# Kernel optimization log

Hardware: AMD Instinct MI355X
Metric: run time of the kernel (lower is better)

## Reference

```python
import jax, jax.numpy as jnp
import numpy as np
import math

PHI = (1 + math.sqrt(5)) / 2
B, T, D, H = 2, 2048, 1024, 16
DH = D // H
DC = 1024
DFF = int(D * PHI)  # 1657


def setup_inputs() -> dict:
    key = jax.random.key(0)
    ks = jax.random.split(key, 16)
    n = lambda i, shape, s=0.02: jax.random.normal(ks[i], shape, jnp.float32) * s
    tril = jnp.tril(jnp.ones((T, T), bool))
    mask = jnp.where(tril, 0.0, -1e9).astype(jnp.float32)[None, None]  # causal additive
    return dict(
        x=jax.random.normal(ks[0], (B, T, D), jnp.float32),
        center_from_above=jax.random.normal(ks[1], (B, DC), jnp.float32),
        mask=mask,
        gate_w=n(2, (D, 1), 0.5), gate_b=jnp.zeros((1,), jnp.float32),
        cb_w=n(3, (DC, 1), 0.5),
        nf_g=jnp.ones((D,), jnp.float32), nf_b=jnp.zeros((D,), jnp.float32),
        wq=n(4, (D, D)), wk=n(5, (D, D)), wv=n(6, (D, D)), wo=n(7, (D, D)),
        phase=jnp.linspace(0.0, math.pi, H).astype(jnp.float32),
        nb_g=jnp.ones((D,), jnp.float32), nb_b=jnp.zeros((D,), jnp.float32),
        up_w=n(8, (D, DFF)), up_b=jnp.zeros((DFF,), jnp.float32),
        dn_w=n(9, (DFF, D)), dn_b=jnp.zeros((D,), jnp.float32),
        commit_w=n(10, (D, 1)), commit_b=jnp.zeros((1,), jnp.float32),
        cproj_w=n(11, (D, DC)), cproj_b=jnp.zeros((DC,), jnp.float32),
        bcast_w=n(12, (DC, D)), bcast_b=jnp.zeros((D,), jnp.float32),
    )


def _ln(x, g, b, eps=1e-5):
    m = x.mean(-1, keepdims=True)
    v = ((x - m) ** 2).mean(-1, keepdims=True)
    return (x - m) * jax.lax.rsqrt(v + eps) * g + b


def _forward(x, center_from_above, mask, gate_w, gate_b, cb_w, nf_g, nf_b,
             wq, wk, wv, wo, phase, nb_g, nb_b, up_w, up_b, dn_w, dn_b,
             commit_w, commit_b, cproj_w, cproj_b, bcast_w, bcast_b):
    # broadcast center from above into the field
    x = x + (center_from_above @ bcast_w + bcast_b)[:, None, :]
    # binary aperture with straight-through estimator
    logits = x @ gate_w + gate_b + (center_from_above @ cb_w)[:, None, :]  # (B,T,1)
    prob = jax.nn.sigmoid(logits)
    hard = (prob > 0.5).astype(x.dtype)
    gate = hard - jax.lax.stop_gradient(prob) + prob
    h = _ln(x, nf_g, nf_b)
    heads = lambda w: (h @ w).reshape(B, T, H, DH).transpose(0, 2, 1, 3)  # (B,H,T,DH)
    Q, K, V = heads(wq), heads(wk), heads(wv)
    half = DH // 2
    c = jnp.cos(phase)[None, :, None, None]
    s = jnp.sin(phase)[None, :, None, None]
    def rot(z):
        re, im = z[..., :half], z[..., half:]
        return jnp.concatenate([re * c - im * s, re * s + im * c], axis=-1)
    Q, K = rot(Q), rot(K)
    ge = gate[:, None]  # (B,1,T,1)
    Q = Q * ge
    K = K * ge
    scores = jnp.einsum('bhqd,bhkd->bhqk', Q, K) / math.sqrt(DH) + mask
    attn = jax.nn.softmax(scores, axis=-1)
    fo = jnp.einsum('bhqk,bhkd->bhqd', attn, V).transpose(0, 2, 1, 3).reshape(B, T, D)
    fo = (fo @ wo) * gate
    x = x + fo
    h2 = _ln(x, nb_g, nb_b)
    ff = jax.nn.gelu(h2 @ up_w + up_b, approximate=False) @ dn_w + dn_b
    center_pool = x.mean(axis=1)  # (B,D)
    commit = jax.nn.sigmoid(center_pool @ commit_w + commit_b)  # (B,1)
    x = x + commit[:, None, :] * gate * ff
    center = jnp.tanh(center_pool @ cproj_w + cproj_b)  # (B,DC)
    return x, center, gate, commit


def reference(x, center_from_above, mask, gate_w, gate_b, cb_w, nf_g, nf_b,
              wq, wk, wv, wo, phase, nb_g, nb_b, up_w, up_b, dn_w, dn_b,
              commit_w, commit_b, cproj_w, cproj_b, bcast_w, bcast_b):
    return _forward(x, center_from_above, mask, gate_w, gate_b, cb_w, nf_g, nf_b,
                    wq, wk, wv, wo, phase, nb_g, nb_b, up_w, up_b, dn_w, dn_b,
                    commit_w, commit_b, cproj_w, cproj_b, bcast_w, bcast_b)
```

## Files before the change

### kernel.cpp

```cpp
#include <hip/hip_runtime.h>
#include <math.h>

#define B_   2
#define T_   2048
#define D_   1024
#define H_   16
#define DH_  64
#define DC_  1024
#define DFF_ 1656
#define DFFP_ 1664
#define MTOT 4096
#define NELEM_X 4194304ull

typedef short s16x8 __attribute__((ext_vector_type(8)));
typedef unsigned short u16x4 __attribute__((ext_vector_type(4)));
typedef float f32x4 __attribute__((ext_vector_type(4)));
typedef float f32x16 __attribute__((ext_vector_type(16)));
typedef unsigned short bfbits;

__device__ __forceinline__ bfbits f2bf(float f) {
  unsigned int u = __builtin_bit_cast(unsigned int, f);
  u += 0x7fffu + ((u >> 16) & 1u);
  return (bfbits)(u >> 16);
}

__device__ __forceinline__ float vexp2(float x) {
  float r;
  asm("v_exp_f32 %0, %1" : "=v"(r) : "v"(x));
  return r;
}
__device__ __forceinline__ unsigned pkbf(float lo, float hi) {
  unsigned r;
  asm("v_cvt_pk_bf16_f32 %0, %1, %2" : "=v"(r) : "v"(lo), "v"(hi));
  return r;
}

__device__ __forceinline__ void gload16(const void* g, void* l) {
  __builtin_amdgcn_global_load_lds(
      (__attribute__((address_space(1))) void*)g,
      (__attribute__((address_space(3))) void*)l, 16, 0, 0);
}

constexpr size_t OFF_X1   = 0;
constexpr size_t OFF_H    = OFF_X1 + 4ull*NELEM_X;
constexpr size_t OFF_Q    = OFF_H  + 2ull*NELEM_X;
constexpr size_t OFF_K    = OFF_Q  + 2ull*NELEM_X;
constexpr size_t OFF_VT   = OFF_K  + 2ull*NELEM_X;
constexpr size_t OFF_AO   = OFF_VT + 2ull*NELEM_X;
constexpr size_t OFF_X2   = OFF_AO + 2ull*NELEM_X;
constexpr size_t OFF_WQKV = OFF_X2 + 4ull*NELEM_X;
constexpr size_t OFF_WO   = OFF_WQKV + 3072ull*1024*2;
constexpr size_t OFF_WUP  = OFF_WO   + 1024ull*1024*2;
constexpr size_t OFF_WDN  = OFF_WUP  + 1664ull*1024*2;
constexpr size_t OFF_BVEC = OFF_WDN  + 1024ull*1664*2;
constexpr size_t OFF_CBV  = OFF_BVEC + 2048ull*4;
constexpr size_t OFF_GATE = OFF_CBV  + 256;
constexpr size_t OFF_PART = OFF_GATE + 4096ull*4;
constexpr size_t OFF_POOL = OFF_PART + 128ull*1024*4;
constexpr size_t OFF_CMT  = OFF_POOL + 2048ull*4;
constexpr size_t OFF_PM   = OFF_CMT  + 256;
constexpr size_t OFF_PL   = OFF_PM   + 1024ull*64*4;

__constant__ unsigned short JOBS[8][6] = {
  {0x00F, 0x11C, 0x11A, 0x118, 0x006, 0x000},
  {0x11E, 0x11D, 0x11B, 0x119, 0x005, 0x001},
  {0x11F, 0x21D, 0x21B, 0x219, 0x004, 0x002},
  {0x21F, 0x21C, 0x00B, 0x114, 0x008, 0x003},
  {0x21E, 0x00C, 0x116, 0x009, 0x007, 0x210},
  {0x00E, 0x117, 0x217, 0x110, 0x111, 0x211},
  {0x00D, 0x218, 0x115, 0x112, 0x213, 0x212},
  {0x21A, 0x215, 0x216, 0x00A, 0x113, 0x214},
};

__global__ __launch_bounds__(256)
void transpose_w(const float* __restrict__ src, bfbits* __restrict__ dst,
                 int R, int C, int Rpad, int Npad) {
  __shared__ float tile[32][33];
  const int kb = blockIdx.x * 32, nb = blockIdx.y * 32;
  const int tx = threadIdx.x & 31, ty = threadIdx.x >> 5;
  for (int i = ty; i < 32; i += 8) {
    const int k = kb + i, n = nb + tx;
    tile[i][tx] = (k < R && n < C) ? src[(size_t)k * C + n] : 0.f;
  }
  __syncthreads();
  for (int i = ty; i < 32; i += 8) {
    const int n = nb + i, k = kb + tx;
    if (n < Npad && k < Rpad) dst[(size_t)n * Rpad + k] = f2bf(tile[tx][i]);
  }
}

__global__ __launch_bounds__(256)
void gemv_t(const float* __restrict__ v, const float* __restrict__ w,
            const float* __restrict__ bias, float* __restrict__ out,
            int tanh_mode) {
  const int b = blockIdx.y;
  const int dl = threadIdx.x & 31, cl = threadIdx.x >> 5;
  const int d = blockIdx.x * 32 + dl;
  const float* vb = v + b * 1024;
  float s = 0.f;
  #pragma unroll 4
  for (int c = cl; c < 1024; c += 8)
    s += vb[c] * w[(size_t)c * 1024 + d];
  __shared__ float red[8][32];
  red[cl][dl] = s;
  __syncthreads();
  if (threadIdx.x < 32) {
    float t = 0.f;
    #pragma unroll
    for (int i = 0; i < 8; ++i) t += red[i][threadIdx.x];
    const int dd = blockIdx.x * 32 + threadIdx.x;
    t += bias[dd];
    out[b * 1024 + dd] = tanh_mode ? tanhf(t) : t;
  }
}

__global__ __launch_bounds__(256)
void cb_kernel(const float* __restrict__ cfa, const float* __restrict__ cbw,
               float* __restrict__ cbv) {
  const int b = blockIdx.x, tid = threadIdx.x;
  float4 a = *(const float4*)(cfa + b * 1024 + tid * 4);
  float4 w = *(const float4*)(cbw + tid * 4);
  float s = a.x * w.x + a.y * w.y + a.z * w.z + a.w * w.w;
  #pragma unroll
  for (int o = 32; o > 0; o >>= 1) s += __shfl_xor(s, o);
  __shared__ float ls[4];
  if ((tid & 63) == 0) ls[tid >> 6] = s;
  __syncthreads();
  if (tid == 0) cbv[b] = ls[0] + ls[1] + ls[2] + ls[3];
}

__device__ __forceinline__ void blockreduce3(float& a, float& b, float& c) {
  #pragma unroll
  for (int o = 32; o > 0; o >>= 1) {
    a += __shfl_xor(a, o);
    b += __shfl_xor(b, o);
    c += __shfl_xor(c, o);
  }
  __shared__ float ls[3][4];
  const int lane = threadIdx.x & 63, w = threadIdx.x >> 6;
  if (lane == 0) { ls[0][w] = a; ls[1][w] = b; ls[2][w] = c; }
  __syncthreads();
  a = ls[0][0] + ls[0][1] + ls[0][2] + ls[0][3];
  b = ls[1][0] + ls[1][1] + ls[1][2] + ls[1][3];
  c = ls[2][0] + ls[2][1] + ls[2][2] + ls[2][3];
}

__global__ __launch_bounds__(256)
void ln1_kernel(const float* __restrict__ x, const float* __restrict__ bvec,
                const float* __restrict__ cbv, const float* __restrict__ gw,
                const float* __restrict__ gb, const float* __restrict__ nfg,
                const float* __restrict__ nfb, float* __restrict__ x1,
                bfbits* __restrict__ h, float* __restrict__ gate_ws,
                float* __restrict__ gate_out) {
  const int m = blockIdx.x, tid = threadIdx.x, b = m >> 11;
  const size_t ro = (size_t)m * D_ + tid * 4;
  float4 xv = *(const float4*)(x + ro);
  float4 bv = *(const float4*)(bvec + b * D_ + tid * 4);
  float4 v;
  v.x = xv.x + bv.x; v.y = xv.y + bv.y; v.z = xv.z + bv.z; v.w = xv.w + bv.w;
  float4 g4 = *(const float4*)(gw + tid * 4);
  float s  = v.x + v.y + v.z + v.w;
  float s2 = v.x*v.x + v.y*v.y + v.z*v.z + v.w*v.w;
  float dg = v.x*g4.x + v.y*g4.y + v.z*g4.z + v.w*g4.w;
  blockreduce3(s, s2, dg);
  const float mean = s * (1.0f/1024.0f);
  const float var  = s2 * (1.0f/1024.0f) - mean*mean;
  const float rstd = rsqrtf(var + 1e-5f);
  if (tid == 0) {
    const float logits = dg + gb[0] + cbv[b];
    const float prob = 1.0f / (1.0f + expf(-logits));
    const float hard = prob > 0.5f ? 1.0f : 0.0f;
    const float gv = (hard - prob) + prob;
    gate_ws[m] = gv; gate_out[m] = gv;
  }
  *(float4*)(x1 + ro) = v;
  float4 gg = *(const float4*)(nfg + tid * 4);
  float4 b2 = *(const float4*)(nfb + tid * 4);
  u16x4 hv;
  hv[0] = f2bf((v.x - mean) * rstd * gg.x + b2.x);
  hv[1] = f2bf((v.y - mean) * rstd * gg.y + b2.y);
  hv[2] = f2bf((v.z - mean) * rstd * gg.z + b2.z);
  hv[3] = f2bf((v.w - mean) * rstd * gg.w + b2.w);
  *(u16x4*)(h + ro) = hv;
}

__global__ __launch_bounds__(256)
void ln2_kernel(const float* __restrict__ x2, const float* __restrict__ gptr,
                const float* __restrict__ bptr, bfbits* __restrict__ h2) {
  const int m = blockIdx.x, tid = threadIdx.x;
  const size_t ro = (size_t)m * D_ + tid * 4;
  float4 v = *(const float4*)(x2 + ro);
  float s  = v.x + v.y + v.z + v.w;
  float s2 = v.x*v.x + v.y*v.y + v.z*v.z + v.w*v.w;
  float d0 = 0.f;
  blockreduce3(s, s2, d0);
  const float mean = s * (1.0f/1024.0f);
  const float var  = s2 * (1.0f/1024.0f) - mean*mean;
  const float rstd = rsqrtf(var + 1e-5f);
  float4 gg = *(const float4*)(gptr + tid * 4);
  float4 b2 = *(const float4*)(bptr + tid * 4);
  u16x4 hv;
  hv[0] = f2bf((v.x - mean) * rstd * gg.x + b2.x);
  hv[1] = f2bf((v.y - mean) * rstd * gg.y + b2.y);
  hv[2] = f2bf((v.z - mean) * rstd * gg.z + b2.z);
  hv[3] = f2bf((v.w - mean) * rstd * gg.w + b2.w);
  *(u16x4*)(h2 + ro) = hv;
}

template <int EPI, int BM, int BK, int BN>
__global__ void __launch_bounds__(256, 2)
gemm_bt(const bfbits* __restrict__ A, int lda,
        const bfbits* __restrict__ Bt, int ldb, int K,
        const float* __restrict__ p0, const float* __restrict__ p1,
        const float* __restrict__ p2,
        float* __restrict__ fo0, const float* __restrict__ fo1,
        bfbits* __restrict__ bo0, bfbits* __restrict__ bo1,
        bfbits* __restrict__ bo2) {
  constexpr int MI = BM / 32;
  constexpr int NJ = BN / 32;
  constexpr int RCH = BK / 8;
  constexpr int NK = BK / 32;
  __shared__ bfbits Asl[2][BM * BK];
  __shared__ bfbits Bsl[2][BN * BK];
  const int tid = threadIdx.x;
  const int lane = tid & 63, wave = tid >> 6;
  const int g = lane >> 4, l15 = lane & 15;
  const int wr = wave >> 1, wc = wave & 1;
  const int m0 = blockIdx.y * BM, n0 = blockIdx.x * BN;

  auto stage = [&](int k0, int p) {
    #pragma unroll
    for (int i = 0; i < (BM * RCH) / 256; ++i) {
      const int c = i * 256 + tid;
      const int row = c / RCH;
      const int ko = ((c % RCH) ^ (row & (RCH - 1))) * 8;
      gload16(A + (size_t)(m0 + row) * lda + (k0 + ko),
              (char*)&Asl[p][0] + c * 16);
    }
    #pragma unroll
    for (int i = 0; i < (BN * RCH) / 256; ++i) {
      const int c = i * 256 + tid;
      const int row = c / RCH;
      const int ko = ((c % RCH) ^ (row & (RCH - 1))) * 8;
      gload16(Bt + (size_t)(n0 + row) * ldb + (k0 + ko),
              (char*)&Bsl[p][0] + c * 16);
    }
  };

  f32x4 acc[MI][NJ] = {};
  stage(0, 0);
  __syncthreads();

  int t = 0;
  for (int k0 = 0; k0 < K; k0 += BK, ++t) {
    const int p = t & 1;
    if (k0 + BK < K) stage(k0 + BK, p ^ 1);
    s16x8 af[NK][MI], bfr[NK][NJ];
    #pragma unroll
    for (int kk = 0; kk < NK; ++kk) {
      #pragma unroll
      for (int i = 0; i < MI; ++i) {
        const int row = wr * (MI * 16) + i * 16 + l15;
        af[kk][i] = *(const s16x8*)&Asl[p][row * BK + (((kk * 4 + g) ^ (row & (RCH - 1))) * 8)];
      }
      #pragma unroll
      for (int i = 0; i < NJ; ++i) {
        const int row = wc * (NJ * 16) + i * 16 + l15;
        bfr[kk][i] = *(const s16x8*)&Bsl[p][row * BK + (((kk * 4 + g) ^ (row & (RCH - 1))) * 8)];
      }
    }
    #pragma unroll
    for (int kk = 0; kk < NK; ++kk)
      #pragma unroll
      for (int i = 0; i < MI; ++i)
        #pragma unroll
        for (int j = 0; j < NJ; ++j)
          acc[i][j] = __builtin_amdgcn_mfma_f32_16x16x32_bf16(af[kk][i], bfr[kk][j], acc[i][j], 0, 0, 0);
    __syncthreads();
  }

  const int b = m0 >> 11;
  const int trow0 = (m0 & 2047) + wr * (MI * 16);

  if constexpr (EPI == 0) {
    const float* gate = p0;
    const float* phase = p1;
    const int ncol0 = n0 + wc * 64;
    const int section = ncol0 >> 10;
    const int hh = (ncol0 & 1023) >> 6;
    if (section == 2) {
      bfbits* vt = bo2;
      const size_t vhead = (size_t)(b * H_ + hh) * DH_ * T_;
      #pragma unroll
      for (int mi = 0; mi < MI; ++mi) {
        const int tb = trow0 + mi * 16 + g * 4;
        #pragma unroll
        for (int ni = 0; ni < NJ; ++ni) {
          const int dh = ni * 16 + l15;
          unsigned* dst32 = (unsigned*)&vt[vhead + (size_t)dh * T_ + tb];
          dst32[0] = pkbf(acc[mi][ni][0], acc[mi][ni][1]);
          dst32[1] = pkbf(acc[mi][ni][2], acc[mi][ni][3]);
        }
      }
    } else {
      const float cc = cosf(phase[hh]);
      const float ssn = sinf(phase[hh]);
      const float qs = (section == 0) ? 0.125f * 1.44269504088896341f : 1.0f;
      bfbits* dst = (section == 0) ? bo0 : bo1;
      const size_t head = (size_t)(b * H_ + hh) * T_ * DH_;
      #pragma unroll
      for (int mi = 0; mi < MI; ++mi) {
        const int tb = trow0 + mi * 16 + g * 4;
        float gv[4];
        #pragma unroll
        for (int r = 0; r < 4; ++r) gv[r] = gate[(size_t)b * T_ + tb + r] * qs;
        #pragma unroll
        for (int ni = 0; ni < 2; ++ni) {
          const int dh = ni * 16 + l15;
          #pragma unroll
          for (int r = 0; r < 4; ++r) {
            const float re = acc[mi][ni][r];
            const float im = acc[mi][ni + 2][r];
            const size_t idx = head + (size_t)(tb + r) * DH_ + dh;
            dst[idx]      = f2bf((re * cc - im * ssn) * gv[r]);
            dst[idx + 32] = f2bf((re * ssn + im * cc) * gv[r]);
          }
        }
      }
    }
  } else if constexpr (EPI == 1) {
    const float* gate = p0;
    const float* x1 = fo1;
    float* x2 = fo0;
    #pragma unroll
    for (int mi = 0; mi < MI; ++mi) {
      const int m = m0 + wr * (MI * 16) + mi * 16 + g * 4;
      float gv[4];
      #pragma unroll
      for (int r = 0; r < 4; ++r) gv[r] = gate[m + r];
      #pragma unroll
      for (int ni = 0; ni < NJ; ++ni) {
        const int n = n0 + wc * (NJ * 16) + ni * 16 + l15;
        #pragma unroll
        for (int r = 0; r < 4; ++r) {
          const size_t idx = (size_t)(m + r) * D_ + n;
          x2[idx] = x1[idx] + acc[mi][ni][r] * gv[r];
        }
      }
    }
  } else if constexpr (EPI == 2) {
    const float* upb = p0;
    bfbits* outm = bo0;
    #pragma unroll
    for (int mi = 0; mi < MI; ++mi) {
      const int m = m0 + wr * (MI * 16) + mi * 16 + g * 4;
      #pragma unroll
      for (int ni = 0; ni < NJ; ++ni) {
        const int n = n0 + wc * (NJ * 16) + ni * 16 + l15;
        const float bb = upb[n < DFF_ ? n : DFF_ - 1];
        #pragma unroll
        for (int r = 0; r < 4; ++r) {
          float v = acc[mi][ni][r] + bb;
          v = 0.5f * v * (1.0f + erff(v * 0.70710678118654752f));
          outm[(size_t)(m + r) * DFFP_ + n] = f2bf(v);
        }
      }
    }
  } else {
    const float* dnb = p0;
    const float* gate = p1;
    const float* cmt = p2;
    const float* x2 = fo1;
    float* outx = fo0;
    const float cb = cmt[b];
    #pragma unroll
    for (int mi = 0; mi < MI; ++mi) {
      const int m = m0 + wr * (MI * 16) + mi * 16 + g * 4;
      float kv[4];
      #pragma unroll
      for (int r = 0; r < 4; ++r) kv[r] = cb * gate[m + r];
      #pragma unroll
      for (int ni = 0; ni < NJ; ++ni) {
        const int n = n0 + wc * (NJ * 16) + ni * 16 + l15;
        const float bb = dnb[n];
        #pragma unroll
        for (int r = 0; r < 4; ++r) {
          const size_t idx = (size_t)(m + r) * D_ + n;
          outx[idx] = x2[idx] + kv[r] * (acc[mi][ni][r] + bb);
        }
      }
    }
  }
}

__global__ void __launch_bounds__(128, 3)
attn_kernel(const bfbits* __restrict__ Qb, const bfbits* __restrict__ Kb,
            const bfbits* __restrict__ Vt, bfbits* __restrict__ AO,
            float* __restrict__ pm, float* __restrict__ pl,
            float* __restrict__ pO) {
  __shared__ bfbits Kl[64 * 64];
  __shared__ bfbits Vl[64 * 64];
  const int pid = blockIdx.x;
  const int bh = pid & 31;
  const int j = (pid >> 5) & 7;
  const int slot = pid >> 8;
  const unsigned job = JOBS[j][slot];
  const int qt = job & 0xFF;
  const int kind = job >> 8;
  const int nk = qt + 1;
  const int mid = (nk + 1) >> 1;
  const int t0 = (kind == 2) ? mid : 0;
  const int t1 = (kind == 1) ? mid : nk;
  const int qb0 = qt * 64;
  const int tid = threadIdx.x, lane = tid & 63, wq = tid >> 6;
  const int l31 = lane & 31, hi = lane >> 5;
  const int qw = qb0 + wq * 32;

  const bfbits* Qp = Qb + ((size_t)bh * T_ + qw) * DH_;
  const bfbits* Kp = Kb + (size_t)bh * T_ * DH_;
  const bfbits* Vp = Vt + (size_t)bh * DH_ * T_;

  s16x8 qf[4];
  #pragma unroll
  for (int mf = 0; mf < 4; ++mf)
    qf[mf] = *(const s16x8*)(Qp + l31 * DH_ + mf * 16 + hi * 8);

  f32x16 o0 = {}, o1 = {};
  float mrun = -INFINITY, lrun = 0.f;

  const bfbits* kg[4];
  const bfbits* vg[4];
  int cb_[4];
  #pragma unroll
  for (int i = 0; i < 4; ++i) {
    const int c = i * 128 + tid;
    const int row = c >> 3;
    const int sc = ((c & 7) ^ (row & 7)) * 8;
    kg[i] = Kp + row * DH_ + sc;
    vg[i] = Vp + (size_t)row * T_ + sc;
    cb_[i] = c * 16;
  }

  for (int t = t0; t < t1; ++t) {
    const int k0 = t << 6;
    #pragma unroll
    for (int i = 0; i < 4; ++i) {
      gload16(kg[i] + (size_t)k0 * DH_, (char*)&Kl[0] + cb_[i]);
      gload16(vg[i] + k0,               (char*)&Vl[0] + cb_[i]);
    }
    __syncthreads();
    f32x16 s0 = {}, s1 = {};
    __builtin_amdgcn_s_setprio(1);
    #pragma unroll
    for (int mf = 0; mf < 4; ++mf) {
      const int ch = ((mf * 2 + hi) ^ (l31 & 7)) * 8;
      const s16x8 ka  = *(const s16x8*)&Kl[l31 * 64 + ch];
      const s16x8 kb2 = *(const s16x8*)&Kl[(32 + l31) * 64 + ch];
      s0 = __builtin_amdgcn_mfma_f32_32x32x16_bf16(ka,  qf[mf], s0, 0, 0, 0);
      s1 = __builtin_amdgcn_mfma_f32_32x32x16_bf16(kb2, qf[mf], s1, 0, 0, 0);
    }
    __builtin_amdgcn_s_setprio(0);
    if (t == qt) {
      const int qd = wq * 32 + l31;
      #pragma unroll
      for (int r = 0; r < 16; ++r) {
        const int krow = (r & 3) + 8 * (r >> 2) + 4 * hi;
        if (krow > qd)      s0[r] = -1e9f;
        if (krow + 32 > qd) s1[r] = -1e9f;
      }
    }
    float red[8];
    #pragma unroll
    for (int i = 0; i < 8; ++i)
      red[i] = fmaxf(fmaxf(s0[i], s0[i + 8]), fmaxf(s1[i], s1[i + 8]));
    #pragma unroll
    for (int i = 0; i < 4; ++i) red[i] = fmaxf(red[i], red[i + 4]);
    float mx = fmaxf(fmaxf(red[0], red[1]), fmaxf(red[2], red[3]));
    mx = fmaxf(mx, __shfl_xor(mx, 32));
    const bool need = __any(mx > mrun + 8.f) != 0;
    const float mnew = need ? fmaxf(mrun, mx) : mrun;
    s0 = s0 - mnew;
    s1 = s1 - mnew;
    #pragma unroll
    for (int i = 0; i < 16; ++i) { s0[i] = vexp2(s0[i]); s1[i] = vexp2(s1[i]); }
    float sr[8];
    #pragma unroll
    for (int i = 0; i < 8; ++i)
      sr[i] = (s0[i] + s0[i + 8]) + (s1[i] + s1[i + 8]);
    #pragma unroll
    for (int i = 0; i < 4; ++i) sr[i] += sr[i + 4];
    float sum = (sr[0] + sr[1]) + (sr[2] + sr[3]);
    sum += __shfl_xor(sum, 32);
    if (need) {
      const float alpha = vexp2(mrun - mnew);
      mrun = mnew;
      lrun = lrun * alpha + sum;
      o0 *= alpha;
      o1 *= alpha;
    } else {
      lrun += sum;
    }
    #pragma unroll
    for (int mf = 0; mf < 4; ++mf) {
      const f32x16& s = (mf < 2) ? s0 : s1;
      const int r0 = (mf & 1) * 8;
      const unsigned A0 = pkbf(s[r0 + 0], s[r0 + 1]);
      const unsigned A1 = pkbf(s[r0 + 2], s[r0 + 3]);
      const unsigned B0 = pkbf(s[r0 + 4], s[r0 + 5]);
      const unsigned B1 = pkbf(s[r0 + 6], s[r0 + 7]);
      const unsigned x0 = (unsigned)__shfl_xor((int)(hi ? A0 : B0), 32);
      const unsigned x1 = (unsigned)__shfl_xor((int)(hi ? A1 : B1), 32);
      uint4 wv;
      wv.x = hi ? x0 : A0;
      wv.y = hi ? x1 : A1;
      wv.z = hi ? B0 : x0;
      wv.w = hi ? B1 : x1;
      const s16x8 pf = __builtin_bit_cast(s16x8, wv);
      const int ch = ((mf * 2 + hi) ^ (l31 & 7)) * 8;
      const s16x8 v0 = *(const s16x8*)&Vl[l31 * 64 + ch];
      const s16x8 v1 = *(const s16x8*)&Vl[(32 + l31) * 64 + ch];
      __builtin_amdgcn_s_setprio(1);
      o0 = __builtin_amdgcn_mfma_f32_32x32x16_bf16(v0, pf, o0, 0, 0, 0);
      o1 = __builtin_amdgcn_mfma_f32_32x32x16_bf16(v1, pf, o1, 0, 0, 0);
      __builtin_amdgcn_s_setprio(0);
    }
    __syncthreads();
  }

  if (kind == 0) {
    const float inv = 1.0f / lrun;
    const int q = qw + l31;
    bfbits* dst = AO + ((size_t)(bh >> 4) * T_ + q) * D_ + (bh & 15) * DH_;
    #pragma unroll
    for (int rp = 0; rp < 8; ++rp) {
      const int dh = ((2 * rp) & 3) + 8 * (rp >> 1) + 4 * hi;
      *(unsigned*)(dst + dh)      = pkbf(o0[2 * rp] * inv, o0[2 * rp + 1] * inv);
      *(unsigned*)(dst + 32 + dh) = pkbf(o1[2 * rp] * inv, o1[2 * rp + 1] * inv);
    }
  } else {
    const int jid = ((qt - 16) * 32 + bh) * 2 + (kind - 1);
    const int qloc = wq * 32 + l31;
    pm[jid * 64 + qloc] = mrun;
    pl[jid * 64 + qloc] = lrun;
    float* po = pO + (size_t)jid * 4096;
    #pragma unroll
    for (int r = 0; r < 16; ++r) {
      const int dh = (r & 3) + 8 * (r >> 2) + 4 * hi;
      po[dh * 64 + qloc]        = o0[r];
      po[(dh + 32) * 64 + qloc] = o1[r];
    }
  }
}

__global__ void __launch_bounds__(64)
attn_merge(const float* __restrict__ pm, const float* __restrict__ pl,
           const float* __restrict__ pO, bfbits* __restrict__ AO) {
  __shared__ float lds[64][65];
  const int u = blockIdx.x;
  const int qt = 16 + (u >> 5), bh = u & 31;
  const int q = threadIdx.x;
  const int jA = ((qt - 16) * 32 + bh) * 2, jB = jA + 1;
  const float mA = pm[jA * 64 + q], mB = pm[jB * 64 + q];
  const float lA = pl[jA * 64 + q], lB = pl[jB * 64 + q];
  const float m = fmaxf(mA, mB);
  const float eA = vexp2(mA - m), eB = vexp2(mB - m);
  const float inv = 1.0f / (lA * eA + lB * eB);
  const float* OA = pO + (size_t)jA * 4096;
  const float* OB = pO + (size_t)jB * 4096;
  for (int dh = 0; dh < 64; ++dh)
    lds[dh][q] = (OA[dh * 64 + q] * eA + OB[dh * 64 + q] * eB) * inv;
  __syncthreads();
  const int b = bh >> 4, hh = bh & 15;
  bfbits* dst = AO + ((size_t)b * T_ + qt * 64) * D_ + hh * DH_ + q;
  for (int qq = 0; qq < 64; ++qq)
    dst[(size_t)qq * D_] = f2bf(lds[q][qq]);
}

__global__ __launch_bounds__(256)
void pool_part(const float* __restrict__ x2, float* __restrict__ part) {
  const int s = blockIdx.x, b = blockIdx.y, tid = threadIdx.x;
  const float* base = x2 + ((size_t)b * T_ + s * 32) * D_ + tid * 4;
  float ax = 0, ay = 0, az = 0, aw = 0;
  #pragma unroll 4
  for (int t = 0; t < 32; ++t) {
    float4 v = *(const float4*)(base + (size_t)t * D_);
    ax += v.x; ay += v.y; az += v.z; aw += v.w;
  }
  float4 ov; ov.x = ax; ov.y = ay; ov.z = az; ov.w = aw;
  *(float4*)(part + (size_t)(b * 64 + s) * D_ + tid * 4) = ov;
}

__global__ __launch_bounds__(256)
void pool_fin(const float* __restrict__ part, float* __restrict__ pool) {
  const int idx = blockIdx.x * 256 + threadIdx.x;
  const int b = idx >> 10, d = idx & 1023;
  float s = 0.f;
  #pragma unroll 8
  for (int i = 0; i < 64; ++i) s += part[(size_t)(b * 64 + i) * D_ + d];
  pool[idx] = s * (1.0f / 2048.0f);
}

__global__ __launch_bounds__(256)
void commit_kernel(const float* __restrict__ pool, const float* __restrict__ cw,
                   const float* __restrict__ cb0, float* __restrict__ cmt,
                   float* __restrict__ out_cmt) {
  const int b = blockIdx.x, tid = threadIdx.x;
  float4 p = *(const float4*)(pool + b * 1024 + tid * 4);
  float4 w = *(const float4*)(cw + tid * 4);
  float s = p.x * w.x + p.y * w.y + p.z * w.z + p.w * w.w;
  #pragma unroll
  for (int o = 32; o > 0; o >>= 1) s += __shfl_xor(s, o);
  __shared__ float ls[4];
  if ((tid & 63) == 0) ls[tid >> 6] = s;
  __syncthreads();
  if (tid == 0) {
    const float t = ls[0] + ls[1] + ls[2] + ls[3] + cb0[0];
    const float v = 1.0f / (1.0f + expf(-t));
    cmt[b] = v; out_cmt[b] = v;
  }
}

extern "C" void kernel_launch(void* const* d_in, const int* in_sizes, int n_in,
                              void* d_out, int out_size, void* d_ws, size_t ws_size,
                              hipStream_t stream) {
  (void)in_sizes; (void)n_in; (void)out_size; (void)ws_size;
  const float* x       = (const float*)d_in[0];
  const float* cfa     = (const float*)d_in[1];
  const float* gate_w  = (const float*)d_in[3];
  const float* gate_b  = (const float*)d_in[4];
  const float* cb_w    = (const float*)d_in[5];
  const float* nf_g    = (const float*)d_in[6];
  const float* nf_b    = (const float*)d_in[7];
  const float* wq      = (const float*)d_in[8];
  const float* wk      = (const float*)d_in[9];
  const float* wv      = (const float*)d_in[10];
  const float* wo      = (const float*)d_in[11];
  const float* phase   = (const float*)d_in[12];
  const float* nb_g    = (const float*)d_in[13];
  const float* nb_b    = (const float*)d_in[14];
  const float* up_w    = (const float*)d_in[15];
  const float* up_b    = (const float*)d_in[16];
  const float* dn_w    = (const float*)d_in[17];
  const float* dn_b    = (const float*)d_in[18];
  const float* cmt_w   = (const float*)d_in[19];
  const float* cmt_b   = (const float*)d_in[20];
  const float* cproj_w = (const float*)d_in[21];
  const float* cproj_b = (const float*)d_in[22];
  const float* bcast_w = (const float*)d_in[23];
  const float* bcast_b = (const float*)d_in[24];

  char* ws = (char*)d_ws;
  float*  x1     = (float*)(ws + OFF_X1);
  bfbits* h      = (bfbits*)(ws + OFF_H);
  bfbits* h2     = (bfbits*)(ws + OFF_H);
  bfbits* qb     = (bfbits*)(ws + OFF_Q);
  bfbits* kb     = (bfbits*)(ws + OFF_K);
  bfbits* vt     = (bfbits*)(ws + OFF_VT);
  bfbits* ffmid  = (bfbits*)(ws + OFF_Q);
  bfbits* ao     = (bfbits*)(ws + OFF_AO);
  float*  x2     = (float*)(ws + OFF_X2);
  float*  pO     = (float*)(ws + OFF_X2);
  bfbits* wqkv_t = (bfbits*)(ws + OFF_WQKV);
  bfbits* wo_t   = (bfbits*)(ws + OFF_WO);
  bfbits* wup_t  = (bfbits*)(ws + OFF_WUP);
  bfbits* wdn_t  = (bfbits*)(ws + OFF_WDN);
  float*  bvec   = (float*)(ws + OFF_BVEC);
  float*  cbv    = (float*)(ws + OFF_CBV);
  float*  gate   = (float*)(ws + OFF_GATE);
  float*  part   = (float*)(ws + OFF_PART);
  float*  pool   = (float*)(ws + OFF_POOL);
  float*  cmt    = (float*)(ws + OFF_CMT);
  float*  pm     = (float*)(ws + OFF_PM);
  float*  pl     = (float*)(ws + OFF_PL);

  float* outx   = (float*)d_out;
  float* outc   = outx + NELEM_X;
  float* outg   = outc + B_ * DC_;
  float* outcmt = outg + B_ * T_;

  transpose_w<<<dim3(32, 32), 256, 0, stream>>>(wq, wqkv_t,                1024, 1024, 1024, 1024);
  transpose_w<<<dim3(32, 32), 256, 0, stream>>>(wk, wqkv_t + 1024 * 1024,  1024, 1024, 1024, 1024);
  transpose_w<<<dim3(32, 32), 256, 0, stream>>>(wv, wqkv_t + 2048 * 1024,  1024, 1024, 1024, 1024);
  transpose_w<<<dim3(32, 32), 256, 0, stream>>>(wo, wo_t,                  1024, 1024, 1024, 1024);
  transpose_w<<<dim3(32, 52), 256, 0, stream>>>(up_w, wup_t,               1024, DFF_, 1024, DFFP_);
  transpose_w<<<dim3(52, 32), 256, 0, stream>>>(dn_w, wdn_t,               DFF_, 1024, DFFP_, 1024);

  gemv_t<<<dim3(32, B_), 256, 0, stream>>>(cfa, bcast_w, bcast_b, bvec, 0);
  cb_kernel<<<B_, 256, 0, stream>>>(cfa, cb_w, cbv);

  ln1_kernel<<<MTOT, 256, 0, stream>>>(x, bvec, cbv, gate_w, gate_b, nf_g, nf_b,
                                       x1, h, gate, outg);

  gemm_bt<0, 128, 32, 128><<<dim3(24, 32), 256, 0, stream>>>(
      h, 1024, wqkv_t, 1024, 1024, gate, phase, nullptr,
      nullptr, nullptr, qb, kb, vt);

  attn_kernel<<<1536, 128, 0, stream>>>(qb, kb, vt, ao, pm, pl, pO);
  attn_merge<<<512, 64, 0, stream>>>(pm, pl, pO, ao);

  gemm_bt<1, 64, 64, 64><<<dim3(16, 64), 256, 0, stream>>>(
      ao, 1024, wo_t, 1024, 1024, gate, nullptr, nullptr,
      x2, x1, nullptr, nullptr, nullptr);

  ln2_kernel<<<MTOT, 256, 0, stream>>>(x2, nb_g, nb_b, h2);

  pool_part<<<dim3(64, B_), 256, 0, stream>>>(x2, part);
  pool_fin<<<8, 256, 0, stream>>>(part, pool);
  commit_kernel<<<B_, 256, 0, stream>>>(pool, cmt_w, cmt_b, cmt, outcmt);
  gemv_t<<<dim3(32, B_), 256, 0, stream>>>(pool, cproj_w, cproj_b, outc, 1);

  gemm_bt<2, 64, 64, 64><<<dim3(26, 64), 256, 0, stream>>>(
      h2, 1024, wup_t, 1024, 1024, up_b, nullptr, nullptr,
      nullptr, nullptr, ffmid, nullptr, nullptr);

  gemm_bt<3, 64, 64, 64><<<dim3(16, 64), 256, 0, stream>>>(
      ffmid, DFFP_, wdn_t, DFFP_, DFFP_, dn_b, gate, cmt,
      outx, x2, nullptr, nullptr, nullptr);
}
```

Measured before the change: 229.5 us.

## Rebalance causal attention split-K schedule, fuse small setup kernels, store partials in bf16

Replaces the old two-way split of late query tiles with a finer job table. Query tiles from 10 upward are split into 2, 3 or 4 key ranges of up to 10 tiles each, and the merge kernel combines a variable number of partials. The partial outputs are stored in bf16 instead of fp32, which halves that traffic but loses some precision. Separately, the six weight-transpose launches become one kernel, bcast-gemv and cb are fused, pool_fin and commit are fused, and the attention occupancy hint rises from 3 to 4 blocks. These cut launch count and tail imbalance at the cost of more merge work and register pressure.

```diff
diff --git a/kernel.cpp b/kernel.cpp
--- a/kernel.cpp
+++ b/kernel.cpp
@@ -22,6 +22,10 @@
   unsigned int u = __builtin_bit_cast(unsigned int, f);
   u += 0x7fffu + ((u >> 16) & 1u);
   return (bfbits)(u >> 16);
+}
+__device__ __forceinline__ float bf2f(bfbits b) {
+  unsigned int u = ((unsigned int)b) << 16;
+  return __builtin_bit_cast(float, u);
 }
 
 __device__ __forceinline__ float vexp2(float x) {
@@ -59,24 +63,57 @@
 constexpr size_t OFF_POOL = OFF_PART + 128ull*1024*4;
 constexpr size_t OFF_CMT  = OFF_POOL + 2048ull*4;
 constexpr size_t OFF_PM   = OFF_CMT  + 256;
-constexpr size_t OFF_PL   = OFF_PM   + 1024ull*64*4;
-
-__constant__ unsigned short JOBS[8][6] = {
-  {0x00F, 0x11C, 0x11A, 0x118, 0x006, 0x000},
-  {0x11E, 0x11D, 0x11B, 0x119, 0x005, 0x001},
-  {0x11F, 0x21D, 0x21B, 0x219, 0x004, 0x002},
-  {0x21F, 0x21C, 0x00B, 0x114, 0x008, 0x003},
-  {0x21E, 0x00C, 0x116, 0x009, 0x007, 0x210},
-  {0x00E, 0x117, 0x217, 0x110, 0x111, 0x211},
-  {0x00D, 0x218, 0x115, 0x112, 0x213, 0x212},
-  {0x21A, 0x215, 0x216, 0x00A, 0x113, 0x214},
+constexpr size_t OFF_PL   = OFF_PM   + 512ull*1024;
+
+#define JB(q,a,b,s) ((unsigned)(q) | ((unsigned)(a)<<8) | ((unsigned)(b)<<16) | ((unsigned)(s)<<24))
+__constant__ unsigned JOBS2[68] = {
+  JB(9,0,10,255),
+  JB(10,0,10,0),  JB(11,0,10,2),  JB(12,0,10,4),  JB(13,0,10,6),
+  JB(14,0,10,8),  JB(15,0,10,10), JB(16,0,10,12), JB(17,0,10,14),
+  JB(18,0,10,16), JB(19,0,10,18), JB(20,0,10,20), JB(21,0,10,23),
+  JB(22,0,10,26), JB(23,0,10,29), JB(24,0,10,32), JB(25,0,10,35),
+  JB(26,0,10,38), JB(27,0,10,41), JB(28,0,10,44), JB(29,0,10,47),
+  JB(30,0,10,50), JB(31,0,10,54),
+  JB(19,10,20,19), JB(20,10,20,21), JB(21,10,20,24), JB(22,10,20,27),
+  JB(23,10,20,30), JB(24,10,20,33), JB(25,10,20,36), JB(26,10,20,39),
+  JB(27,10,20,42), JB(28,10,20,45), JB(29,10,20,48), JB(30,10,20,51),
+  JB(31,10,20,55),
+  JB(29,20,30,49), JB(30,20,30,52), JB(31,20,30,56),
+  JB(8,0,9,255),  JB(18,10,19,17), JB(28,20,29,46),
+  JB(7,0,8,255),  JB(17,10,18,15), JB(27,20,28,43),
+  JB(6,0,7,255),  JB(16,10,17,13), JB(26,20,27,40),
+  JB(5,0,6,255),  JB(15,10,16,11), JB(25,20,26,37),
+  JB(4,0,5,255),  JB(14,10,15,9),  JB(24,20,25,34),
+  JB(3,0,4,255),  JB(13,10,14,7),  JB(23,20,24,31),
+  JB(2,0,3,255),  JB(12,10,13,5),  JB(22,20,23,28),
+  JB(1,0,2,255),  JB(11,10,12,3),  JB(21,20,22,25), JB(31,30,32,57),
+  JB(0,0,1,255),  JB(10,10,11,1),  JB(20,20,21,22), JB(30,30,31,53),
 };
 
 __global__ __launch_bounds__(256)
-void transpose_w(const float* __restrict__ src, bfbits* __restrict__ dst,
-                 int R, int C, int Rpad, int Npad) {
+void transpose_all(const float* __restrict__ wq, const float* __restrict__ wk,
+                   const float* __restrict__ wv, const float* __restrict__ wo,
+                   const float* __restrict__ up, const float* __restrict__ dn,
+                   char* __restrict__ ws) {
+  const int bid = blockIdx.x;
+  const float* src;
+  bfbits* dst;
+  int R, C, Rpad, Npad, gw, loc;
+  if (bid < 4096) {
+    R = C = Rpad = Npad = 1024; gw = 32;
+    const int j = bid >> 10; loc = bid & 1023;
+    src = (j == 0) ? wq : (j == 1) ? wk : (j == 2) ? wv : wo;
+    dst = (j < 3) ? (bfbits*)(ws + OFF_WQKV) + (size_t)j * 1024 * 1024
+                  : (bfbits*)(ws + OFF_WO);
+  } else if (bid < 5760) {
+    R = 1024; C = DFF_; Rpad = 1024; Npad = DFFP_; gw = 32; loc = bid - 4096;
+    src = up; dst = (bfbits*)(ws + OFF_WUP);
+  } else {
+    R = DFF_; C = 1024; Rpad = DFFP_; Npad = 1024; gw = 52; loc = bid - 5760;
+    src = dn; dst = (bfbits*)(ws + OFF_WDN);
+  }
+  const int kb = (loc % gw) * 32, nb = (loc / gw) * 32;
   __shared__ float tile[32][33];
-  const int kb = blockIdx.x * 32, nb = blockIdx.y * 32;
   const int tx = threadIdx.x & 31, ty = threadIdx.x >> 5;
   for (int i = ty; i < 32; i += 8) {
     const int k = kb + i, n = nb + tx;
@@ -90,9 +127,45 @@
 }
 
 __global__ __launch_bounds__(256)
+void bvec_cb_kernel(const float* __restrict__ cfa, const float* __restrict__ bw,
+                    const float* __restrict__ bb, const float* __restrict__ cbw,
+                    float* __restrict__ bvec, float* __restrict__ cbv) {
+  const int b = blockIdx.y;
+  if (blockIdx.x == 32) {
+    const int tid = threadIdx.x;
+    float4 a = *(const float4*)(cfa + b * 1024 + tid * 4);
+    float4 w = *(const float4*)(cbw + tid * 4);
+    float s = a.x * w.x + a.y * w.y + a.z * w.z + a.w * w.w;
+    #pragma unroll
+    for (int o = 32; o > 0; o >>= 1) s += __shfl_xor(s, o);
+    __shared__ float ls[4];
+    if ((tid & 63) == 0) ls[tid >> 6] = s;
+    __syncthreads();
+    if (tid == 0) cbv[b] = ls[0] + ls[1] + ls[2] + ls[3];
+    return;
+  }
+  const int dl = threadIdx.x & 31, cl = threadIdx.x >> 5;
+  const int d = blockIdx.x * 32 + dl;
+  const float* vb = cfa + b * 1024;
+  float s = 0.f;
+  #pragma unroll 4
+  for (int c = cl; c < 1024; c += 8)
+    s += vb[c] * bw[(size_t)c * 1024 + d];
+  __shared__ float red[8][32];
+  red[cl][dl] = s;
+  __syncthreads();
+  if (threadIdx.x < 32) {
+    float t = 0.f;
+    #pragma unroll
+    for (int i = 0; i < 8; ++i) t += red[i][threadIdx.x];
+    const int dd = blockIdx.x * 32 + threadIdx.x;
+    bvec[b * 1024 + dd] = t + bb[dd];
+  }
+}
+
+__global__ __launch_bounds__(256)
 void gemv_t(const float* __restrict__ v, const float* __restrict__ w,
-            const float* __restrict__ bias, float* __restrict__ out,
-            int tanh_mode) {
+            const float* __restrict__ bias, float* __restrict__ out) {
   const int b = blockIdx.y;
   const int dl = threadIdx.x & 31, cl = threadIdx.x >> 5;
   const int d = blockIdx.x * 32 + dl;
@@ -109,24 +182,8 @@
     #pragma unroll
     for (int i = 0; i < 8; ++i) t += red[i][threadIdx.x];
     const int dd = blockIdx.x * 32 + threadIdx.x;
-    t += bias[dd];
-    out[b * 1024 + dd] = tanh_mode ? tanhf(t) : t;
-  }
-}
-
-__global__ __launch_bounds__(256)
-void cb_kernel(const float* __restrict__ cfa, const float* __restrict__ cbw,
-               float* __restrict__ cbv) {
-  const int b = blockIdx.x, tid = threadIdx.x;
-  float4 a = *(const float4*)(cfa + b * 1024 + tid * 4);
-  float4 w = *(const float4*)(cbw + tid * 4);
-  float s = a.x * w.x + a.y * w.y + a.z * w.z + a.w * w.w;
-  #pragma unroll
-  for (int o = 32; o > 0; o >>= 1) s += __shfl_xor(s, o);
-  __shared__ float ls[4];
-  if ((tid & 63) == 0) ls[tid >> 6] = s;
-  __syncthreads();
-  if (tid == 0) cbv[b] = ls[0] + ls[1] + ls[2] + ls[3];
+    out[b * 1024 + dd] = tanhf(t + bias[dd]);
+  }
 }
 
 __device__ __forceinline__ void blockreduce3(float& a, float& b, float& c) {
@@ -393,24 +450,20 @@
   }
 }
 
-__global__ void __launch_bounds__(128, 3)
+__global__ void __launch_bounds__(128, 4)
 attn_kernel(const bfbits* __restrict__ Qb, const bfbits* __restrict__ Kb,
             const bfbits* __restrict__ Vt, bfbits* __restrict__ AO,
             float* __restrict__ pm, float* __restrict__ pl,
-            float* __restrict__ pO) {
+            bfbits* __restrict__ pO) {
   __shared__ bfbits Kl[64 * 64];
   __shared__ bfbits Vl[64 * 64];
   const int pid = blockIdx.x;
   const int bh = pid & 31;
-  const int j = (pid >> 5) & 7;
-  const int slot = pid >> 8;
-  const unsigned job = JOBS[j][slot];
+  const unsigned job = JOBS2[pid >> 5];
   const int qt = job & 0xFF;
-  const int kind = job >> 8;
-  const int nk = qt + 1;
-  const int mid = (nk + 1) >> 1;
-  const int t0 = (kind == 2) ? mid : 0;
-  const int t1 = (kind == 1) ? mid : nk;
+  const int t0 = (job >> 8) & 0xFF;
+  const int t1 = (job >> 16) & 0xFF;
+  const int js = job >> 24;
   const int qb0 = qt * 64;
   const int tid = threadIdx.x, lane = tid & 63, wq = tid >> 6;
   const int l31 = lane & 31, hi = lane >> 5;
@@ -527,7 +580,7 @@
     __syncthreads();
   }
 
-  if (kind == 0) {
+  if (js == 255) {
     const float inv = 1.0f / lrun;
     const int q = qw + l31;
     bfbits* dst = AO + ((size_t)(bh >> 4) * T_ + q) * D_ + (bh & 15) * DH_;
@@ -538,37 +591,50 @@
       *(unsigned*)(dst + 32 + dh) = pkbf(o1[2 * rp] * inv, o1[2 * rp + 1] * inv);
     }
   } else {
-    const int jid = ((qt - 16) * 32 + bh) * 2 + (kind - 1);
+    const int jid = bh * 58 + js;
     const int qloc = wq * 32 + l31;
     pm[jid * 64 + qloc] = mrun;
     pl[jid * 64 + qloc] = lrun;
-    float* po = pO + (size_t)jid * 4096;
+    bfbits* po = pO + (size_t)jid * 4096;
     #pragma unroll
     for (int r = 0; r < 16; ++r) {
       const int dh = (r & 3) + 8 * (r >> 2) + 4 * hi;
-      po[dh * 64 + qloc]        = o0[r];
-      po[(dh + 32) * 64 + qloc] = o1[r];
+      po[dh * 64 + qloc]        = f2bf(o0[r]);
+      po[(dh + 32) * 64 + qloc] = f2bf(o1[r]);
     }
   }
 }
 
 __global__ void __launch_bounds__(64)
 attn_merge(const float* __restrict__ pm, const float* __restrict__ pl,
-           const float* __restrict__ pO, bfbits* __restrict__ AO) {
+           const bfbits* __restrict__ pO, bfbits* __restrict__ AO) {
   __shared__ float lds[64][65];
   const int u = blockIdx.x;
-  const int qt = 16 + (u >> 5), bh = u & 31;
+  const int qt = 10 + (u >> 5), bh = u & 31;
   const int q = threadIdx.x;
-  const int jA = ((qt - 16) * 32 + bh) * 2, jB = jA + 1;
-  const float mA = pm[jA * 64 + q], mB = pm[jB * 64 + q];
-  const float lA = pl[jA * 64 + q], lB = pl[jB * 64 + q];
-  const float m = fmaxf(mA, mB);
-  const float eA = vexp2(mA - m), eB = vexp2(mB - m);
-  const float inv = 1.0f / (lA * eA + lB * eB);
-  const float* OA = pO + (size_t)jA * 4096;
-  const float* OB = pO + (size_t)jB * 4096;
-  for (int dh = 0; dh < 64; ++dh)
-    lds[dh][q] = (OA[dh * 64 + q] * eA + OB[dh * 64 + q] * eB) * inv;
+  const int P = (qt + 10) / 10;
+  const int pbase = (qt < 20) ? (qt - 10) * 2
+                  : (qt < 30) ? 20 + (qt - 20) * 3
+                              : 50 + (qt - 30) * 4;
+  const int jb = bh * 58 + pbase;
+  float mv[4], ev[4];
+  float m = -INFINITY;
+  for (int p = 0; p < P; ++p) {
+    mv[p] = pm[(jb + p) * 64 + q];
+    m = fmaxf(m, mv[p]);
+  }
+  float l = 0.f;
+  for (int p = 0; p < P; ++p) {
+    ev[p] = vexp2(mv[p] - m);
+    l += pl[(jb + p) * 64 + q] * ev[p];
+  }
+  const float inv = 1.0f / l;
+  for (int dh = 0; dh < 64; ++dh) {
+    float acc = 0.f;
+    for (int p = 0; p < P; ++p)
+      acc += bf2f(pO[(size_t)(jb + p) * 4096 + dh * 64 + q]) * ev[p];
+    lds[dh][q] = acc * inv;
+  }
   __syncthreads();
   const int b = bh >> 4, hh = bh & 15;
   bfbits* dst = AO + ((size_t)b * T_ + qt * 64) * D_ + hh * DH_ + q;
@@ -591,23 +657,23 @@
 }
 
 __global__ __launch_bounds__(256)
-void pool_fin(const float* __restrict__ part, float* __restrict__ pool) {
-  const int idx = blockIdx.x * 256 + threadIdx.x;
-  const int b = idx >> 10, d = idx & 1023;
-  float s = 0.f;
+void pool_fin_commit(const float* __restrict__ part, const float* __restrict__ cw,
+                     const float* __restrict__ cb0, float* __restrict__ pool,
+                     float* __restrict__ cmt, float* __restrict__ out_cmt) {
+  const int b = blockIdx.x, tid = threadIdx.x;
+  const int d0 = tid * 4;
+  float ax = 0, ay = 0, az = 0, aw = 0;
   #pragma unroll 8
-  for (int i = 0; i < 64; ++i) s += part[(size_t)(b * 64 + i) * D_ + d];
-  pool[idx] = s * (1.0f / 2048.0f);
-}
-
-__global__ __launch_bounds__(256)
-void commit_kernel(const float* __restrict__ pool, const float* __restrict__ cw,
-                   const float* __restrict__ cb0, float* __restrict__ cmt,
-                   float* __restrict__ out_cmt) {
-  const int b = blockIdx.x, tid = threadIdx.x;
-  float4 p = *(const float4*)(pool + b * 1024 + tid * 4);
-  float4 w = *(const float4*)(cw + tid * 4);
-  float s = p.x * w.x + p.y * w.y + p.z * w.z + p.w * w.w;
+  for (int i = 0; i < 64; ++i) {
+    float4 v = *(const float4*)(part + (size_t)(b * 64 + i) * D_ + d0);
+    ax += v.x; ay += v.y; az += v.z; aw += v.w;
+  }
+  ax *= (1.0f / 2048.0f); ay *= (1.0f / 2048.0f);
+  az *= (1.0f / 2048.0f); aw *= (1.0f / 2048.0f);
+  float4 ov; ov.x = ax; ov.y = ay; ov.z = az; ov.w = aw;
+  *(float4*)(pool + b * 1024 + d0) = ov;
+  float4 w = *(const float4*)(cw + d0);
+  float s = ax * w.x + ay * w.y + az * w.z + aw * w.w;
   #pragma unroll
   for (int o = 32; o > 0; o >>= 1) s += __shfl_xor(s, o);
   __shared__ float ls[4];
@@ -659,7 +725,7 @@
   bfbits* ffmid  = (bfbits*)(ws + OFF_Q);
   bfbits* ao     = (bfbits*)(ws + OFF_AO);
   float*  x2     = (float*)(ws + OFF_X2);
-  float*  pO     = (float*)(ws + OFF_X2);
+  bfbits* pO     = (bfbits*)(ws + OFF_X2);
   bfbits* wqkv_t = (bfbits*)(ws + OFF_WQKV);
   bfbits* wo_t   = (bfbits*)(ws + OFF_WO);
   bfbits* wup_t  = (bfbits*)(ws + OFF_WUP);
@@ -678,15 +744,10 @@
   float* outg   = outc + B_ * DC_;
   float* outcmt = outg + B_ * T_;
 
-  transpose_w<<<dim3(32, 32), 256, 0, stream>>>(wq, wqkv_t,                1024, 1024, 1024, 1024);
-  transpose_w<<<dim3(32, 32), 256, 0, stream>>>(wk, wqkv_t + 1024 * 1024,  1024, 1024, 1024, 1024);
-  transpose_w<<<dim3(32, 32), 256, 0, stream>>>(wv, wqkv_t + 2048 * 1024,  1024, 1024, 1024, 1024);
-  transpose_w<<<dim3(32, 32), 256, 0, stream>>>(wo, wo_t,                  1024, 1024, 1024, 1024);
-  transpose_w<<<dim3(32, 52), 256, 0, stream>>>(up_w, wup_t,               1024, DFF_, 1024, DFFP_);
-  transpose_w<<<dim3(52, 32), 256, 0, stream>>>(dn_w, wdn_t,               DFF_, 1024, DFFP_, 1024);
-
-  gemv_t<<<dim3(32, B_), 256, 0, stream>>>(cfa, bcast_w, bcast_b, bvec, 0);
-  cb_kernel<<<B_, 256, 0, stream>>>(cfa, cb_w, cbv);
+  transpose_all<<<7424, 256, 0, stream>>>(wq, wk, wv, wo, up_w, dn_w, ws);
+
+  bvec_cb_kernel<<<dim3(33, B_), 256, 0, stream>>>(cfa, bcast_w, bcast_b, cb_w,
+                                                   bvec, cbv);
 
   ln1_kernel<<<MTOT, 256, 0, stream>>>(x, bvec, cbv, gate_w, gate_b, nf_g, nf_b,
                                        x1, h, gate, outg);
@@ -695,8 +756,8 @@
       h, 1024, wqkv_t, 1024, 1024, gate, phase, nullptr,
       nullptr, nullptr, qb, kb, vt);
 
-  attn_kernel<<<1536, 128, 0, stream>>>(qb, kb, vt, ao, pm, pl, pO);
-  attn_merge<<<512, 64, 0, stream>>>(pm, pl, pO, ao);
+  attn_kernel<<<2176, 128, 0, stream>>>(qb, kb, vt, ao, pm, pl, pO);
+  attn_merge<<<704, 64, 0, stream>>>(pm, pl, pO, ao);
 
   gemm_bt<1, 64, 64, 64><<<dim3(16, 64), 256, 0, stream>>>(
       ao, 1024, wo_t, 1024, 1024, gate, nullptr, nullptr,
@@ -705,9 +766,8 @@
   ln2_kernel<<<MTOT, 256, 0, stream>>>(x2, nb_g, nb_b, h2);
 
   pool_part<<<dim3(64, B_), 256, 0, stream>>>(x2, part);
-  pool_fin<<<8, 256, 0, stream>>>(part, pool);
-  commit_kernel<<<B_, 256, 0, stream>>>(pool, cmt_w, cmt_b, cmt, outcmt);
-  gemv_t<<<dim3(32, B_), 256, 0, stream>>>(pool, cproj_w, cproj_b, outc, 1);
+  pool_fin_commit<<<B_, 256, 0, stream>>>(part, cmt_w, cmt_b, pool, cmt, outcmt);
+  gemv_t<<<dim3(32, B_), 256, 0, stream>>>(pool, cproj_w, cproj_b, outc);
 
   gemm_bt<2, 64, 64, 64><<<dim3(26, 64), 256, 0, stream>>>(
       h2, 1024, wup_t, 1024, 1024, up_b, nullptr, nullptr,
```

Measured after the change: 294.8 us. 1.28x slower.
